# Kernel tuning notes

Hardware: AMD Instinct MI355X
Metric: run time of the kernel (lower is better)

The kernel has to match this reference:

```python
import jax, jax.numpy as jnp
import numpy as np

BF, SEQ, DIM = 8, 1024, 640
HEADS, HEAD_DIM = 8, 80
CTX, CROSS = 77, 768

def layer_norm(x, g, b, eps=1e-5):
    mu = x.mean(-1, keepdims=True)
    var = ((x - mu) ** 2).mean(-1, keepdims=True)
    return (x - mu) * jax.lax.rsqrt(var + eps) * g + b

def mha(q, k, v):
    # q: [B, Sq, DIM], k/v: [B, Sk, DIM]
    B, Sq, _ = q.shape
    scale = jnp.asarray(HEAD_DIM, q.dtype) ** -0.5
    qh = q.reshape(B, Sq, HEADS, HEAD_DIM).transpose(0, 2, 1, 3)
    kh = k.reshape(B, -1, HEADS, HEAD_DIM).transpose(0, 2, 1, 3)
    vh = v.reshape(B, -1, HEADS, HEAD_DIM).transpose(0, 2, 1, 3)
    scores = jnp.einsum('bhqd,bhkd->bhqk', qh, kh) * scale
    probs = jax.nn.softmax(scores, axis=-1)
    out = jnp.einsum('bhqk,bhkd->bhqd', probs, vh)
    return out.transpose(0, 2, 1, 3).reshape(B, Sq, HEADS * HEAD_DIM)

def sparse_causal_kv(x, f):
    # x: [(b f), d, c] -> [(b f), 2d, c]: concat frame-0 KV with previous-frame KV
    b = x.shape[0] // f
    x = x.reshape(b, f, x.shape[1], x.shape[2])
    first = jnp.broadcast_to(x[:, :1], x.shape)
    former_idx = jnp.maximum(np.arange(f) - 1, 0)
    former = x[:, former_idx]
    out = jnp.concatenate([first, former], axis=2)  # [b, f, 2d, c]
    return out.reshape(b * f, -1, x.shape[-1])


def setup_inputs() -> dict:
    key = jax.random.key(0)
    ks = jax.random.split(key, 16)
    s = lambda d: 1.0 / np.sqrt(d)
    inp = {
        'hidden_states': jax.random.normal(ks[0], (BF, SEQ, DIM), jnp.float32),
        'encoder_hidden_states': jax.random.normal(ks[1], (BF, CTX, CROSS), jnp.float32),
        'n1_g': jnp.ones((DIM,), jnp.float32), 'n1_b': jnp.zeros((DIM,), jnp.float32),
        'q1': jax.random.normal(ks[2], (DIM, DIM), jnp.float32) * s(DIM),
        'k1': jax.random.normal(ks[3], (DIM, DIM), jnp.float32) * s(DIM),
        'v1': jax.random.normal(ks[4], (DIM, DIM), jnp.float32) * s(DIM),
        'o1': jax.random.normal(ks[5], (DIM, DIM), jnp.float32) * s(DIM),
        'o1_b': jnp.zeros((DIM,), jnp.float32),
        'n2_g': jnp.ones((DIM,), jnp.float32), 'n2_b': jnp.zeros((DIM,), jnp.float32),
        'q2': jax.random.normal(ks[6], (DIM, DIM), jnp.float32) * s(DIM),
        'k2': jax.random.normal(ks[7], (CROSS, DIM), jnp.float32) * s(CROSS),
        'v2': jax.random.normal(ks[8], (CROSS, DIM), jnp.float32) * s(CROSS),
        'o2': jax.random.normal(ks[9], (DIM, DIM), jnp.float32) * s(DIM),
        'o2_b': jnp.zeros((DIM,), jnp.float32),
        'n3_g': jnp.ones((DIM,), jnp.float32), 'n3_b': jnp.zeros((DIM,), jnp.float32),
        'ff1': jax.random.normal(ks[10], (DIM, 2 * 4 * DIM), jnp.float32) * s(DIM),
        'ff1_b': jnp.zeros((2 * 4 * DIM,), jnp.float32),
        'ff2': jax.random.normal(ks[11], (4 * DIM, DIM), jnp.float32) * s(4 * DIM),
        'ff2_b': jnp.zeros((DIM,), jnp.float32),
        'video_length': 8,
    }
    return inp


def reference(hidden_states, encoder_hidden_states, n1_g, n1_b, q1, k1, v1, o1, o1_b,
              n2_g, n2_b, q2, k2, v2, o2, o2_b, n3_g, n3_b, ff1, ff1_b, ff2, ff2_b,
              video_length):
    hs = hidden_states
    # --- attn1: sparse-causal self-attention ---
    n = layer_norm(hs, n1_g, n1_b)
    q = n @ q1
    k = sparse_causal_kv(n @ k1, video_length)
    v = sparse_causal_kv(n @ v1, video_length)
    hs = mha(q, k, v) @ o1 + o1_b + hs
    # --- attn2: cross-attention to text context ---
    n = layer_norm(hs, n2_g, n2_b)
    a = mha(n @ q2, encoder_hidden_states @ k2, encoder_hidden_states @ v2)
    hs = a @ o2 + o2_b + hs
    # --- GEGLU feed-forward ---
    n = layer_norm(hs, n3_g, n3_b)
    proj = n @ ff1 + ff1_b
    x, gate = jnp.split(proj, 2, axis=-1)
    hs = (x * jax.nn.gelu(gate, approximate=False)) @ ff2 + ff2_b + hs
    return hs
```

## Files before the change

### kernel.cpp

```cpp
#include <hip/hip_runtime.h>
#include <hip/hip_bf16.h>
#include <cmath>

typedef __attribute__((ext_vector_type(8))) short short8;
typedef __attribute__((ext_vector_type(4))) short short4v;
typedef __attribute__((ext_vector_type(4))) float floatx4;

static __device__ __forceinline__ float b2f(__hip_bfloat16 x) { return __bfloat162float(x); }
static __device__ __forceinline__ __hip_bfloat16 f2b(float x) { return __float2bfloat16(x); }
static __device__ __forceinline__ short f2bs(float x) {
    __hip_bfloat16 h = __float2bfloat16(x);
    return __builtin_bit_cast(short, h);
}

static __device__ __forceinline__ float gelu_exact(float x) {
    const float z = x * 0.70710678118654752440f;
    const float a = fabsf(z);
    const float t = __frcp_rn(1.0f + 0.3275911f * a);
    float p = 1.061405429f;
    p = p * t - 1.453152027f;
    p = p * t + 1.421413741f;
    p = p * t - 0.284496736f;
    p = p * t + 0.254829592f;
    p = p * t;
    const float e = __expf(-a * a);
    float erfa = 1.0f - p * e;
    erfa = copysignf(erfa, z);
    return 0.5f * x * (1.0f + erfa);
}

static __device__ __forceinline__ void gl_lds16(const void* g, unsigned ldsoff) {
    __builtin_amdgcn_global_load_lds(
        (const __attribute__((address_space(1))) void*)(unsigned long long)(size_t)g,
        (__attribute__((address_space(3))) void*)(unsigned long long)ldsoff, 16, 0, 0);
}

__global__ void k_detect(const unsigned* __restrict__ g1, int* __restrict__ flag) {
    if (threadIdx.x == 0 && blockIdx.x == 0) {
        *flag = (*g1 == 0x3F800000u) ? 1 : 0;
    }
}

struct CvDesc { const void* src; __hip_bfloat16* dst; int n; int blk0; };
struct CvPack { CvDesc d[12]; };

__global__ __launch_bounds__(256) void k_convert_batch(CvPack P, const int* __restrict__ flag) {
    const bool isf = (*flag != 0);
    const int bid = blockIdx.x;
    int seg = 0;
#pragma unroll
    for (int i = 1; i < 12; ++i)
        if (bid >= P.d[i].blk0) seg = i;
    const CvDesc D = P.d[seg];
    const int i0 = (bid - D.blk0) * 1024 + threadIdx.x * 4;
    if (i0 >= D.n) return;
    if (isf) {
        const float* s = (const float*)D.src;
        if (i0 + 3 < D.n) {
            const float4 v = *(const float4*)(s + i0);
            short4v o4;
            o4[0] = f2bs(v.x); o4[1] = f2bs(v.y); o4[2] = f2bs(v.z); o4[3] = f2bs(v.w);
            *(short4v*)((short*)D.dst + i0) = o4;
        } else {
            for (int j = i0; j < D.n; ++j) D.dst[j] = f2b(s[j]);
        }
    } else {
        const short* s = (const short*)D.src;
        if (i0 + 3 < D.n) {
            *(short4v*)((short*)D.dst + i0) = *(const short4v*)(s + i0);
        } else {
            for (int j = i0; j < D.n; ++j) ((short*)D.dst)[j] = s[j];
        }
    }
}

struct TrDesc { const void* src; __hip_bfloat16* dst; int R; int C; int nbx; int blk0; };
struct TrPack { TrDesc d[10]; };

__global__ void k_transpose_batch(TrPack P, const int* __restrict__ flag) {
    const bool isf = (*flag != 0);
    __shared__ __hip_bfloat16 tile[32][33];
    const int bid = blockIdx.x;
    int seg = 0;
#pragma unroll
    for (int i = 1; i < 10; ++i)
        if (bid >= P.d[i].blk0) seg = i;
    const TrDesc D = P.d[seg];
    const int local = bid - D.blk0;
    const int c0 = (local % D.nbx) * 32, r0 = (local / D.nbx) * 32;
    const int tx = threadIdx.x, ty = threadIdx.y;
    for (int i = ty; i < 32; i += 8) {
        const size_t idx = (size_t)(r0 + i) * D.C + (c0 + tx);
        tile[i][tx] = isf ? f2b(((const float*)D.src)[idx]) : ((const __hip_bfloat16*)D.src)[idx];
    }
    __syncthreads();
    for (int i = ty; i < 32; i += 8)
        D.dst[(size_t)(c0 + i) * D.R + (r0 + tx)] = tile[tx][i];
}

__global__ __launch_bounds__(256) void k_layernorm(const __hip_bfloat16* __restrict__ x,
                                                   const __hip_bfloat16* __restrict__ g,
                                                   const __hip_bfloat16* __restrict__ b,
                                                   __hip_bfloat16* __restrict__ out) {
    const int w = threadIdx.x >> 6, l = threadIdx.x & 63;
    const int row = blockIdx.x * 4 + w;
    const __hip_bfloat16* xr = x + (size_t)row * 640;
    float v[10];
    float s1 = 0.f, s2 = 0.f;
#pragma unroll
    for (int i = 0; i < 10; ++i) {
        v[i] = b2f(xr[l + i * 64]);
        s1 += v[i]; s2 += v[i] * v[i];
    }
#pragma unroll
    for (int mk = 1; mk <= 32; mk <<= 1) {
        s1 += __shfl_xor(s1, mk, 64);
        s2 += __shfl_xor(s2, mk, 64);
    }
    const float mu = s1 * (1.f / 640.f);
    const float var = s2 * (1.f / 640.f) - mu * mu;
    const float rstd = rsqrtf(var + 1e-5f);
    __hip_bfloat16* orow = out + (size_t)row * 640;
#pragma unroll
    for (int i = 0; i < 10; ++i) {
        const int c = l + i * 64;
        orow[c] = f2b((v[i] - mu) * rstd * b2f(g[c]) + b2f(b[c]));
    }
}

template <int MODE>
__global__ __launch_bounds__(256, 2) void k_gemm_big(const __hip_bfloat16* __restrict__ A,
                                                     const __hip_bfloat16* __restrict__ Bt,
                                                     const __hip_bfloat16* __restrict__ bias,
                                                     const __hip_bfloat16* res,
                                                     __hip_bfloat16* outb, float* outf,
                                                     const int* __restrict__ flag,
                                                     int M, int N, int K) {
    __shared__ __align__(16) short lds[16384];
    const bool isf = (MODE == 2) ? (*flag != 0) : false;
    const int t = threadIdx.x;
    const int w = t >> 6, l = t & 63;
    const int quad = l >> 4, l16 = l & 15;
    const int wr = (w >> 1) * 64, wc = (w & 1) * 64;
    const int m0 = blockIdx.y * 128, n0 = blockIdx.x * 128;

    const int srow = t >> 2;
    const int scol = ((t & 3) ^ ((srow >> 1) & 3)) * 8;
    int ar0 = m0 + srow;       if (ar0 >= M) ar0 = M - 1;
    int ar1 = m0 + 64 + srow;  if (ar1 >= M) ar1 = M - 1;
    const __hip_bfloat16* ga0 = A + (size_t)ar0 * K + scol;
    const __hip_bfloat16* ga1 = A + (size_t)ar1 * K + scol;
    const __hip_bfloat16* gb0 = Bt + (size_t)(n0 + srow) * K + scol;
    const __hip_bfloat16* gb1 = Bt + (size_t)(n0 + 64 + srow) * K + scol;
    const unsigned ldsbase = (unsigned)(size_t)&lds[0];
    const unsigned stA0 = ldsbase + (unsigned)(w * 64) * 16;
    const unsigned stA1 = stA0 + 4096;
    const unsigned stB0 = ldsbase + 8192 + (unsigned)(w * 64) * 16;
    const unsigned stB1 = stB0 + 4096;

    const int rsw = (quad ^ ((l16 >> 1) & 3)) * 8;

    floatx4 acc[4][4];
#pragma unroll
    for (int i = 0; i < 4; ++i)
#pragma unroll
        for (int j = 0; j < 4; ++j) acc[i][j] = floatx4{0.f, 0.f, 0.f, 0.f};

    gl_lds16(ga0, stA0);
    gl_lds16(ga1, stA1);
    gl_lds16(gb0, stB0);
    gl_lds16(gb1, stB1);
    __syncthreads();

    int cur = 0;
    for (int k0 = 0; k0 < K; k0 += 32) {
        const int kn = k0 + 32;
        if (kn < K) {
            const unsigned off = (unsigned)(cur ^ 1) * 16384u;
            gl_lds16(ga0 + kn, stA0 + off);
            gl_lds16(ga1 + kn, stA1 + off);
            gl_lds16(gb0 + kn, stB0 + off);
            gl_lds16(gb1 + kn, stB1 + off);
        }
        const int cb = cur * 8192;
        short8 af[4], bf[4];
#pragma unroll
        for (int mt = 0; mt < 4; ++mt)
            af[mt] = *(const short8*)&lds[cb + (wr + mt * 16 + l16) * 32 + rsw];
#pragma unroll
        for (int nt = 0; nt < 4; ++nt)
            bf[nt] = *(const short8*)&lds[cb + 4096 + (wc + nt * 16 + l16) * 32 + rsw];
#pragma unroll
        for (int mt = 0; mt < 4; ++mt)
#pragma unroll
            for (int nt = 0; nt < 4; ++nt)
                acc[mt][nt] = __builtin_amdgcn_mfma_f32_16x16x32_bf16(af[mt], bf[nt], acc[mt][nt], 0, 0, 0);
        __syncthreads();
        cur ^= 1;
    }

#pragma unroll
    for (int mt = 0; mt < 4; ++mt)
#pragma unroll
        for (int nt = 0; nt < 4; ++nt)
#pragma unroll
            for (int r = 0; r < 4; ++r) {
                const int row = m0 + wr + mt * 16 + quad * 4 + r;
                if (row >= M) continue;
                const int col = n0 + wc + nt * 16 + l16;
                float v = acc[mt][nt][r];
                if (bias) v += b2f(bias[col]);
                const size_t idx = (size_t)row * N + col;
                if constexpr (MODE == 0) {
                    outb[idx] = f2b(v);
                } else if constexpr (MODE == 4) {
                    outb[idx] = f2b(col < 640 ? v * 0.16129851867f : v);
                } else if constexpr (MODE == 1) {
                    outb[idx] = f2b(v + b2f(res[idx]));
                } else {
                    v += b2f(res[idx]);
                    if (isf) outf[idx] = v; else outb[idx] = f2b(v);
                }
            }
}

__global__ __launch_bounds__(256, 2) void k_glu_big(const __hip_bfloat16* __restrict__ A,
                                                    const __hip_bfloat16* __restrict__ Bt,
                                                    const __hip_bfloat16* __restrict__ bias,
                                                    __hip_bfloat16* __restrict__ outp,
                                                    int M, int Nh, int K) {
    __shared__ __align__(16) short lds[24576];
    const int t = threadIdx.x;
    const int w = t >> 6, l = t & 63;
    const int quad = l >> 4, l16 = l & 15;
    const int wr = (w >> 1) * 64, wc = (w & 1) * 64;
    const int m0 = blockIdx.y * 128, n0 = blockIdx.x * 128;

    const int srow = t >> 2;
    const int scol = ((t & 3) ^ ((srow >> 1) & 3)) * 8;
    const __hip_bfloat16* ga0 = A + (size_t)(m0 + srow) * K + scol;
    const __hip_bfloat16* ga1 = A + (size_t)(m0 + 64 + srow) * K + scol;
    const __hip_bfloat16* gx0 = Bt + (size_t)(n0 + srow) * K + scol;
    const __hip_bfloat16* gx1 = Bt + (size_t)(n0 + 64 + srow) * K + scol;
    const __hip_bfloat16* gg0 = Bt + (size_t)(Nh + n0 + srow) * K + scol;
    const __hip_bfloat16* gg1 = Bt + (size_t)(Nh + n0 + 64 + srow) * K + scol;
    const unsigned ldsbase = (unsigned)(size_t)&lds[0];
    const unsigned stA0 = ldsbase + (unsigned)(w * 64) * 16;
    const unsigned stA1 = stA0 + 4096;
    const unsigned stX0 = ldsbase + 8192 + (unsigned)(w * 64) * 16;
    const unsigned stX1 = stX0 + 4096;
    const unsigned stG0 = ldsbase + 16384 + (unsigned)(w * 64) * 16;
    const unsigned stG1 = stG0 + 4096;

    const int rsw = (quad ^ ((l16 >> 1) & 3)) * 8;

    floatx4 ax[4][4], ag[4][4];
#pragma unroll
    for (int i = 0; i < 4; ++i)
#pragma unroll
        for (int j = 0; j < 4; ++j) {
            ax[i][j] = floatx4{0.f, 0.f, 0.f, 0.f};
            ag[i][j] = floatx4{0.f, 0.f, 0.f, 0.f};
        }

    gl_lds16(ga0, stA0); gl_lds16(ga1, stA1);
    gl_lds16(gx0, stX0); gl_lds16(gx1, stX1);
    gl_lds16(gg0, stG0); gl_lds16(gg1, stG1);
    __syncthreads();

    int cur = 0;
    for (int k0 = 0; k0 < K; k0 += 32) {
        const int kn = k0 + 32;
        if (kn < K) {
            const unsigned off = (unsigned)(cur ^ 1) * 24576u;
            gl_lds16(ga0 + kn, stA0 + off); gl_lds16(ga1 + kn, stA1 + off);
            gl_lds16(gx0 + kn, stX0 + off); gl_lds16(gx1 + kn, stX1 + off);
            gl_lds16(gg0 + kn, stG0 + off); gl_lds16(gg1 + kn, stG1 + off);
        }
        const int cb = cur * 12288;
        short8 af[4], bxf[4], bgf[4];
#pragma unroll
        for (int mt = 0; mt < 4; ++mt)
            af[mt] = *(const short8*)&lds[cb + (wr + mt * 16 + l16) * 32 + rsw];
#pragma unroll
        for (int nt = 0; nt < 4; ++nt) {
            bxf[nt] = *(const short8*)&lds[cb + 4096 + (wc + nt * 16 + l16) * 32 + rsw];
            bgf[nt] = *(const short8*)&lds[cb + 8192 + (wc + nt * 16 + l16) * 32 + rsw];
        }
#pragma unroll
        for (int mt = 0; mt < 4; ++mt)
#pragma unroll
            for (int nt = 0; nt < 4; ++nt) {
                ax[mt][nt] = __builtin_amdgcn_mfma_f32_16x16x32_bf16(af[mt], bxf[nt], ax[mt][nt], 0, 0, 0);
                ag[mt][nt] = __builtin_amdgcn_mfma_f32_16x16x32_bf16(af[mt], bgf[nt], ag[mt][nt], 0, 0, 0);
            }
        __syncthreads();
        cur ^= 1;
    }

#pragma unroll
    for (int mt = 0; mt < 4; ++mt)
#pragma unroll
        for (int nt = 0; nt < 4; ++nt)
#pragma unroll
            for (int r = 0; r < 4; ++r) {
                const int row = m0 + wr + mt * 16 + quad * 4 + r;
                const int col = n0 + wc + nt * 16 + l16;
                float xv = ax[mt][nt][r] + b2f(bias[col]);
                float gv = ag[mt][nt][r] + b2f(bias[Nh + col]);
                outp[(size_t)row * Nh + col] = f2b(xv * gelu_exact(gv));
            }
}

template <int MODE>
__global__ __launch_bounds__(256) void k_gemm128(const __hip_bfloat16* __restrict__ A,
                                                 const __hip_bfloat16* __restrict__ Bt,
                                                 const __hip_bfloat16* __restrict__ bias,
                                                 const __hip_bfloat16* res,
                                                 __hip_bfloat16* outb, float* outf,
                                                 const int* __restrict__ flag,
                                                 int M, int N, int K) {
    __shared__ __align__(16) short lds[12288];
    const bool isf = (MODE == 2) ? (*flag != 0) : false;
    const int t = threadIdx.x;
    const int w = t >> 6, l = t & 63;
    const int quad = l >> 4, l16 = l & 15;
    const int m0 = blockIdx.y * 128, n0 = blockIdx.x * 64;

    const int chunk = w * 64 + l;
    const int srow = chunk >> 2;
    const int scol = ((chunk & 3) ^ ((srow >> 1) & 3)) * 8;
    int ar0 = m0 + srow;       if (ar0 >= M) ar0 = M - 1;
    int ar1 = m0 + 64 + srow;  if (ar1 >= M) ar1 = M - 1;
    const __hip_bfloat16* ga0 = A + (size_t)ar0 * K + scol;
    const __hip_bfloat16* ga1 = A + (size_t)ar1 * K + scol;
    const __hip_bfloat16* gb  = Bt + (size_t)(n0 + srow) * K + scol;
    const unsigned ldsbase = (unsigned)(size_t)&lds[0];
    const unsigned stA0 = ldsbase + (unsigned)(w * 64) * 16;
    const unsigned stA1 = stA0 + 4096;
    const unsigned stB  = ldsbase + 8192 + (unsigned)(w * 64) * 16;

    const int rsw = (quad ^ ((l16 >> 1) & 3)) * 8;

    floatx4 acc[2][4];
#pragma unroll
    for (int i = 0; i < 2; ++i)
#pragma unroll
        for (int j = 0; j < 4; ++j) acc[i][j] = floatx4{0.f, 0.f, 0.f, 0.f};

    gl_lds16(ga0, stA0);
    gl_lds16(ga1, stA1);
    gl_lds16(gb, stB);
    __syncthreads();

    int cur = 0;
    for (int k0 = 0; k0 < K; k0 += 32) {
        const int kn = k0 + 32;
        if (kn < K) {
            const unsigned off = (unsigned)(cur ^ 1) * 12288u;
            gl_lds16(ga0 + kn, stA0 + off);
            gl_lds16(ga1 + kn, stA1 + off);
            gl_lds16(gb + kn, stB + off);
        }
        const int cb = cur * 6144;
        short8 af[2], bf[4];
#pragma unroll
        for (int mt = 0; mt < 2; ++mt)
            af[mt] = *(const short8*)&lds[cb + (w * 32 + mt * 16 + l16) * 32 + rsw];
#pragma unroll
        for (int nt = 0; nt < 4; ++nt)
            bf[nt] = *(const short8*)&lds[cb + 4096 + (nt * 16 + l16) * 32 + rsw];
#pragma unroll
        for (int mt = 0; mt < 2; ++mt)
#pragma unroll
            for (int nt = 0; nt < 4; ++nt)
                acc[mt][nt] = __builtin_amdgcn_mfma_f32_16x16x32_bf16(af[mt], bf[nt], acc[mt][nt], 0, 0, 0);
        __syncthreads();
        cur ^= 1;
    }

    if constexpr (MODE == 3) {
        short* vt = (short*)outb;
#pragma unroll
        for (int half = 0; half < 2; ++half) {
            __syncthreads();
#pragma unroll
            for (int nn = 0; nn < 2; ++nn) {
                const int nt = half * 2 + nn;
#pragma unroll
                for (int mt = 0; mt < 2; ++mt)
#pragma unroll
                    for (int r = 0; r < 4; ++r)
                        lds[(nn * 16 + l16) * 136 + w * 32 + mt * 16 + quad * 4 + r] =
                            f2bs(acc[mt][nt][r]);
            }
            __syncthreads();
            for (int c = t; c < 512; c += 256) {
                const int cl = c >> 4, seg = c & 15;
                const int col = n0 + half * 32 + cl;
                const int hh = col / 80, dd = col % 80;
                const int row0 = m0 + seg * 8;
                const int f = row0 >> 10, tok = row0 & 1023;
                short8 v8;
#pragma unroll
                for (int j = 0; j < 8; ++j) v8[j] = lds[cl * 136 + seg * 8 + j];
                *(short8*)(vt + (((size_t)((f * 8 + hh) * 80 + dd)) << 10) + tok) = v8;
            }
        }
        return;
    }

#pragma unroll
    for (int mt = 0; mt < 2; ++mt)
#pragma unroll
        for (int nt = 0; nt < 4; ++nt)
#pragma unroll
            for (int r = 0; r < 4; ++r) {
                const int row = m0 + w * 32 + mt * 16 + quad * 4 + r;
                if (row >= M) continue;
                const int col = n0 + nt * 16 + l16;
                float v = acc[mt][nt][r];
                if (bias) v += b2f(bias[col]);
                const size_t idx = (size_t)row * N + col;
                if constexpr (MODE == 0) {
                    outb[idx] = f2b(v);
                } else if constexpr (MODE == 1) {
                    outb[idx] = f2b(v + b2f(res[idx]));
                } else {
                    v += b2f(res[idx]);
                    if (isf) outf[idx] = v; else outb[idx] = f2b(v);
                }
            }
}

__global__ __launch_bounds__(256) void k_attn_self(const __hip_bfloat16* __restrict__ qk,
                                                   const __hip_bfloat16* __restrict__ vt,
                                                   __hip_bfloat16* __restrict__ o) {
    constexpr int KS_OFF = 0;
    constexpr int VT_OFF = 5632;
    constexpr int PS_OFF = 11712;
    constexpr int QS = 1280;
    __shared__ __align__(16) short lds[16576];
    const int t = threadIdx.x;
    const int wave = t >> 6, lane = t & 63, quad = lane >> 4, l16 = lane & 15;
    const int bid = blockIdx.x;
    const int h = bid & 7, qt = (bid >> 3) & 15, b = bid >> 7;
    const int f1 = (b > 0) ? (b - 1) : 0;
    const int nkt = (b < 2) ? 16 : 32;

    for (int i = t; i < 512; i += 256) lds[KS_OFF + (i >> 3) * 88 + 80 + (i & 7)] = 0;

    int kgo[3], klo[3], vgo[3], vlo[3];
#pragma unroll
    for (int j = 0; j < 3; ++j) {
        const int c = t + j * 256;
        const int krow = c / 10, kseg = c % 10;
        kgo[j] = krow * QS + kseg * 8;
        klo[j] = KS_OFF + krow * 88 + kseg * 8;
        const int vd = c >> 3, vseg = c & 7;
        vgo[j] = (vd << 10) + vseg * 8;
        vlo[j] = VT_OFF + vd * 76 + vseg * 8;
    }
    const int nj = (t < 128) ? 3 : 2;

    short8 qf[3];
    {
        const short* qp = (const short*)(qk + ((size_t)(b * 1024 + qt * 64 + wave * 16 + l16)) * QS + h * 80);
#pragma unroll
        for (int ks = 0; ks < 3; ++ks) {
            const int d0 = ks * 32 + quad * 8;
            qf[ks] = (d0 < 80) ? *(const short8*)(qp + d0) : short8{0, 0, 0, 0, 0, 0, 0, 0};
        }
    }

    floatx4 oacc[5];
#pragma unroll
    for (int dt = 0; dt < 5; ++dt) oacc[dt] = floatx4{0.f, 0.f, 0.f, 0.f};
    float lsum[4] = {0.f, 0.f, 0.f, 0.f};

    const short* kb0 = (const short*)qk + 640 + h * 80;
    const short* vb0 = (const short*)vt + (((size_t)h * 80) << 10);

    short8 kreg[3], vreg[3];
    {
#pragma unroll
        for (int j = 0; j < 3; ++j)
            if (j < nj) {
                kreg[j] = *(const short8*)(kb0 + kgo[j]);
                vreg[j] = *(const short8*)(vb0 + vgo[j]);
            }
#pragma unroll
        for (int j = 0; j < 3; ++j)
            if (j < nj) {
                *(short8*)&lds[klo[j]] = kreg[j];
                *(short8*)&lds[vlo[j]] = vreg[j];
            }
    }
    __syncthreads();

    for (int kt = 0; kt < nkt; ++kt) {
        const bool more = (kt + 1 < nkt);
        if (more) {
            const int kn = kt + 1;
            const int fr = (kn < 16) ? 0 : f1;
            const int tok0 = (kn < 16) ? kn * 64 : (kn - 16) * 64;
            const short* kbase = kb0 + (size_t)(fr * 1024 + tok0) * QS;
            const short* vtb = vb0 + (((size_t)(fr * 640)) << 10) + tok0;
#pragma unroll
            for (int j = 0; j < 3; ++j)
                if (j < nj) {
                    kreg[j] = *(const short8*)(kbase + kgo[j]);
                    vreg[j] = *(const short8*)(vtb + vgo[j]);
                }
        }

        floatx4 sv[4];
        __builtin_amdgcn_s_setprio(1);
#pragma unroll
        for (int nt = 0; nt < 4; ++nt) {
            floatx4 acc = {0.f, 0.f, 0.f, 0.f};
#pragma unroll
            for (int ks = 0; ks < 3; ++ks) {
                short8 bf = *(const short8*)&lds[KS_OFF + (nt * 16 + l16) * 88 + ks * 32 + quad * 8];
                acc = __builtin_amdgcn_mfma_f32_16x16x32_bf16(qf[ks], bf, acc, 0, 0, 0);
            }
            sv[nt] = acc;
        }
        __builtin_amdgcn_s_setprio(0);

#pragma unroll
        for (int nt = 0; nt < 4; ++nt) {
#pragma unroll
            for (int r = 0; r < 4; ++r) {
                const float pv = __builtin_amdgcn_exp2f(fminf(sv[nt][r], 115.f));
                lsum[r] += pv;
                lds[PS_OFF + wave * 1216 + (quad * 4 + r) * 76 + nt * 16 + l16] = f2bs(pv);
            }
        }

        __builtin_amdgcn_s_setprio(1);
#pragma unroll
        for (int ks = 0; ks < 2; ++ks) {
            short8 pf = *(const short8*)&lds[PS_OFF + wave * 1216 + l16 * 76 + ks * 32 + quad * 8];
#pragma unroll
            for (int dt = 0; dt < 5; ++dt) {
                short8 vf = *(const short8*)&lds[VT_OFF + (dt * 16 + l16) * 76 + ks * 32 + quad * 8];
                oacc[dt] = __builtin_amdgcn_mfma_f32_16x16x32_bf16(pf, vf, oacc[dt], 0, 0, 0);
            }
        }
        __builtin_amdgcn_s_setprio(0);

        if (more) {
            __syncthreads();
#pragma unroll
            for (int j = 0; j < 3; ++j)
                if (j < nj) {
                    *(short8*)&lds[klo[j]] = kreg[j];
                    *(short8*)&lds[vlo[j]] = vreg[j];
                }
            __syncthreads();
        }
    }

#pragma unroll
    for (int mk = 1; mk <= 8; mk <<= 1)
#pragma unroll
        for (int r = 0; r < 4; ++r)
            lsum[r] += __shfl_xor(lsum[r], mk, 64);

    const int orow = b * 1024 + qt * 64 + wave * 16 + quad * 4;
#pragma unroll
    for (int r = 0; r < 4; ++r) {
        const float inv = 1.f / lsum[r];
        __hip_bfloat16* op = o + (size_t)(orow + r) * 640 + h * 80 + l16;
#pragma unroll
        for (int dt = 0; dt < 5; ++dt)
            op[dt * 16] = f2b(oacc[dt][r] * inv);
    }
}

__global__ __launch_bounds__(256) void k_attn_cross(const __hip_bfloat16* __restrict__ q,
                                                    const __hip_bfloat16* __restrict__ kv,
                                                    __hip_bfloat16* __restrict__ o) {
    constexpr int KS_OFF = 0;
    constexpr int VT_OFF = 7040;
    constexpr int PS_OFF = 15360;
    __shared__ __align__(16) short lds[22016];
    const int t = threadIdx.x;
    const int wave = t >> 6, lane = t & 63, quad = lane >> 4, l16 = lane & 15;
    const int qt = blockIdx.x, h = blockIdx.y, b = blockIdx.z;
    const float scale = 0.11180339887498949f;

    for (int c = t; c < 2752; c += 256) *(short8*)&lds[c * 8] = short8{0, 0, 0, 0, 0, 0, 0, 0};
    __syncthreads();

    const short* kb = (const short*)(kv + (size_t)(b * 77) * 1280 + h * 80);
    const short* vb = (const short*)(kv + (size_t)(b * 77) * 1280 + 640 + h * 80);
    for (int c = t; c < 770; c += 256) {
        const int r = c / 10, seg = c % 10;
        *(short8*)&lds[KS_OFF + r * 88 + seg * 8] = *(const short8*)(kb + (size_t)r * 1280 + seg * 8);
        short8 v8 = *(const short8*)(vb + (size_t)r * 1280 + seg * 8);
#pragma unroll
        for (int j = 0; j < 8; ++j)
            lds[VT_OFF + (seg * 8 + j) * 104 + r] = v8[j];
    }
    short8 qf[3];
    {
        const short* qp = (const short*)(q + ((size_t)(b * 1024 + qt * 64 + wave * 16 + l16)) * 640 + h * 80);
#pragma unroll
        for (int ks = 0; ks < 3; ++ks) {
            const int d0 = ks * 32 + quad * 8;
            qf[ks] = (d0 < 80) ? *(const short8*)(qp + d0) : short8{0, 0, 0, 0, 0, 0, 0, 0};
        }
    }
    __syncthreads();

    floatx4 sv[5];
#pragma unroll
    for (int nt = 0; nt < 5; ++nt) {
        floatx4 acc = {0.f, 0.f, 0.f, 0.f};
#pragma unroll
        for (int ks = 0; ks < 3; ++ks) {
            short8 bf = *(const short8*)&lds[KS_OFF + (nt * 16 + l16) * 88 + ks * 32 + quad * 8];
            acc = __builtin_amdgcn_mfma_f32_16x16x32_bf16(qf[ks], bf, acc, 0, 0, 0);
        }
        sv[nt] = acc;
    }

    float rs[4] = {0.f, 0.f, 0.f, 0.f};
#pragma unroll
    for (int nt = 0; nt < 5; ++nt) {
#pragma unroll
        for (int r = 0; r < 4; ++r) {
            float pv = __expf(fminf(sv[nt][r] * scale, 80.f));
            if (nt == 4 && l16 >= 13) pv = 0.f;
            rs[r] += pv;
            lds[PS_OFF + wave * 1664 + (quad * 4 + r) * 104 + nt * 16 + l16] = f2bs(pv);
        }
    }
#pragma unroll
    for (int mk = 1; mk <= 8; mk <<= 1)
#pragma unroll
        for (int r = 0; r < 4; ++r)
            rs[r] += __shfl_xor(rs[r], mk, 64);

    floatx4 oacc[5];
#pragma unroll
    for (int dt = 0; dt < 5; ++dt) oacc[dt] = floatx4{0.f, 0.f, 0.f, 0.f};
#pragma unroll
    for (int ks = 0; ks < 3; ++ks) {
        short8 pf = *(const short8*)&lds[PS_OFF + wave * 1664 + l16 * 104 + ks * 32 + quad * 8];
#pragma unroll
        for (int dt = 0; dt < 5; ++dt) {
            short8 vf = *(const short8*)&lds[VT_OFF + (dt * 16 + l16) * 104 + ks * 32 + quad * 8];
            oacc[dt] = __builtin_amdgcn_mfma_f32_16x16x32_bf16(pf, vf, oacc[dt], 0, 0, 0);
        }
    }

    const int orow = b * 1024 + qt * 64 + wave * 16 + quad * 4;
#pragma unroll
    for (int r = 0; r < 4; ++r) {
        const float inv = 1.f / rs[r];
        __hip_bfloat16* op = o + (size_t)(orow + r) * 640 + h * 80 + l16;
#pragma unroll
        for (int dt = 0; dt < 5; ++dt)
            op[dt * 16] = f2b(oacc[dt][r] * inv);
    }
}

extern "C" void kernel_launch(void* const* d_in, const int* in_sizes, int n_in,
                              void* d_out, int out_size, void* d_ws, size_t ws_size,
                              hipStream_t stream) {
    char* p = (char*)d_ws;
    auto carve = [&](size_t bytes) -> void* {
        void* r = (void*)p;
        p += (bytes + 255) & ~(size_t)255;
        return r;
    };
    const size_t MD = (size_t)8192 * 640;
    int*            flag  = (int*)carve(256);
    __hip_bfloat16* resid = (__hip_bfloat16*)carve(MD * 2);
    __hip_bfloat16* nb    = (__hip_bfloat16*)carve(MD * 2);
    __hip_bfloat16* qkb   = (__hip_bfloat16*)carve((size_t)8192 * 1280 * 2);
    __hip_bfloat16* vtb   = (__hip_bfloat16*)carve((size_t)64 * 80 * 1024 * 2);
    __hip_bfloat16* ehsb  = (__hip_bfloat16*)carve((size_t)616 * 768 * 2);
    __hip_bfloat16* kvctx = (__hip_bfloat16*)carve((size_t)616 * 1280 * 2);
    __hip_bfloat16* qk1t  = (__hip_bfloat16*)carve((size_t)1280 * 640 * 2);
    __hip_bfloat16* v1t   = (__hip_bfloat16*)carve((size_t)640 * 640 * 2);
    __hip_bfloat16* kv2t  = (__hip_bfloat16*)carve((size_t)1280 * 768 * 2);
    __hip_bfloat16* q2t   = (__hip_bfloat16*)carve((size_t)640 * 640 * 2);
    __hip_bfloat16* o1t   = (__hip_bfloat16*)carve((size_t)640 * 640 * 2);
    __hip_bfloat16* o2t   = (__hip_bfloat16*)carve((size_t)640 * 640 * 2);
    __hip_bfloat16* ff1t  = (__hip_bfloat16*)carve((size_t)5120 * 640 * 2);
    __hip_bfloat16* ff2t  = (__hip_bfloat16*)carve((size_t)640 * 2560 * 2);
    __hip_bfloat16* bpool = (__hip_bfloat16*)carve((size_t)10880 * 2);
    __hip_bfloat16* n1g = bpool, *n1b = bpool + 640, *n2g = bpool + 1280, *n2b = bpool + 1920;
    __hip_bfloat16* n3g = bpool + 2560, *n3b = bpool + 3200, *o1b = bpool + 3840, *o2b = bpool + 4480;
    __hip_bfloat16* f1b = bpool + 5120, *f2b_ = bpool + 10240;

    const size_t hb_bytes = (size_t)8192 * 2560 * 2;
    __hip_bfloat16* hb = nullptr;
    {
        size_t used = (size_t)(p - (char*)d_ws);
        if (ws_size >= used + hb_bytes + 1024) hb = (__hip_bfloat16*)carve(hb_bytes);
    }

    k_detect<<<1, 64, 0, stream>>>((const unsigned*)d_in[2], flag);

    {
        CvPack P;
        auto set = [&](int i, const void* s, __hip_bfloat16* d, int n, int& blk) {
            P.d[i].src = s; P.d[i].dst = d; P.d[i].n = n; P.d[i].blk0 = blk;
            blk += (n + 1023) / 1024;
        };
        int blk = 0;
        set(0,  d_in[0],  resid, (int)MD, blk);
        set(1,  d_in[1],  ehsb, 616 * 768, blk);
        set(2,  d_in[2],  n1g, 640, blk);
        set(3,  d_in[3],  n1b, 640, blk);
        set(4,  d_in[9],  n2g, 640, blk);
        set(5,  d_in[10], n2b, 640, blk);
        set(6,  d_in[16], n3g, 640, blk);
        set(7,  d_in[17], n3b, 640, blk);
        set(8,  d_in[8],  o1b, 640, blk);
        set(9,  d_in[15], o2b, 640, blk);
        set(10, d_in[19], f1b, 5120, blk);
        set(11, d_in[21], f2b_, 640, blk);
        k_convert_batch<<<blk, 256, 0, stream>>>(P, flag);
    }

    {
        TrPack P;
        auto set = [&](int i, const void* s, __hip_bfloat16* d, int R, int C, int& blk) {
            P.d[i].src = s; P.d[i].dst = d; P.d[i].R = R; P.d[i].C = C;
            P.d[i].nbx = C / 32; P.d[i].blk0 = blk;
            blk += (C / 32) * (R / 32);
        };
        int blk = 0;
        set(0, d_in[4],  qk1t,             640, 640, blk);
        set(1, d_in[5],  qk1t + 640 * 640, 640, 640, blk);
        set(2, d_in[6],  v1t,  640, 640, blk);
        set(3, d_in[7],  o1t,  640, 640, blk);
        set(4, d_in[11], q2t,  640, 640, blk);
        set(5, d_in[12], kv2t,             768, 640, blk);
        set(6, d_in[13], kv2t + 640 * 768, 768, 640, blk);
        set(7, d_in[14], o2t,  640, 640, blk);
        set(8, d_in[18], ff1t, 640, 5120, blk);
        set(9, d_in[20], ff2t, 2560, 640, blk);
        k_transpose_batch<<<blk, dim3(32, 8), 0, stream>>>(P, flag);
    }

    k_layernorm<<<2048, 256, 0, stream>>>(resid, n1g, n1b, nb);
    k_gemm_big<4><<<dim3(10, 64), 256, 0, stream>>>(nb, qk1t, nullptr, nullptr, qkb, nullptr, flag,
                                                    8192, 1280, 640);
    k_gemm128<3><<<dim3(10, 64), 256, 0, stream>>>(nb, v1t, nullptr, nullptr, vtb, nullptr, flag,
                                                   8192, 640, 640);
    k_attn_self<<<1024, 256, 0, stream>>>(qkb, vtb, nb);
    k_gemm128<1><<<dim3(10, 64), 256, 0, stream>>>(nb, o1t, o1b, resid, resid, nullptr, flag,
                                                   8192, 640, 640);

    k_layernorm<<<2048, 256, 0, stream>>>(resid, n2g, n2b, nb);
    k_gemm128<0><<<dim3(10, 64), 256, 0, stream>>>(nb, q2t, nullptr, nullptr, qkb, nullptr, flag,
                                                   8192, 640, 640);
    k_gemm128<0><<<dim3(20, 5), 256, 0, stream>>>(ehsb, kv2t, nullptr, nullptr, kvctx, nullptr, flag,
                                                  616, 1280, 768);
    k_attn_cross<<<dim3(16, 8, 8), 256, 0, stream>>>(qkb, kvctx, nb);
    k_gemm128<1><<<dim3(10, 64), 256, 0, stream>>>(nb, o2t, o2b, resid, resid, nullptr, flag,
                                                   8192, 640, 640);

    k_layernorm<<<2048, 256, 0, stream>>>(resid, n3g, n3b, nb);
    if (hb) {
        k_glu_big<<<dim3(20, 64), 256, 0, stream>>>(nb, ff1t, f1b, hb, 8192, 2560, 640);
        k_gemm128<2><<<dim3(10, 64), 256, 0, stream>>>(hb, ff2t, f2b_, resid,
                                                       (__hip_bfloat16*)d_out, (float*)d_out, flag,
                                                       8192, 640, 2560);
    } else {
        for (int c = 0; c < 2; ++c) {
            const size_t off = (size_t)c * 4096 * 640;
            k_glu_big<<<dim3(20, 32), 256, 0, stream>>>(nb + off, ff1t, f1b, qkb, 4096, 2560, 640);
            k_gemm128<2><<<dim3(5, 32), 256, 0, stream>>>(qkb, ff2t, f2b_, resid + off,
                                                          (__hip_bfloat16*)d_out + off,
                                                          (float*)d_out + off, flag,
                                                          4096, 640, 2560);
        }
    }
    (void)in_sizes; (void)n_in; (void)out_size;
}
```

Baseline: 537.8 us.

## Split QK^T across waves by key columns and share probabilities via LDS

Each wave now holds Q fragments for all 64 query rows and computes scores against its own 16-key slice. The resulting probabilities are written to a shared LDS tile that all waves read for the PV product. Row sums are combined across waves through LDS before normalisation. This cuts per-wave K fragment loads from LDS, but adds a block barrier per key tile and quadruples the Q register footprint.

```diff
diff --git a/kernel.cpp b/kernel.cpp
--- a/kernel.cpp
+++ b/kernel.cpp
@@ -463,20 +463,26 @@
     }
     const int nj = (t < 128) ? 3 : 2;
 
-    short8 qf[3];
-    {
-        const short* qp = (const short*)(qk + ((size_t)(b * 1024 + qt * 64 + wave * 16 + l16)) * QS + h * 80);
+    short8 qf[4][3];
+#pragma unroll
+    for (int g = 0; g < 4; ++g) {
+        const short* qp = (const short*)(qk +
+            ((size_t)(b * 1024 + qt * 64 + g * 16 + l16)) * QS + h * 80);
 #pragma unroll
         for (int ks = 0; ks < 3; ++ks) {
             const int d0 = ks * 32 + quad * 8;
-            qf[ks] = (d0 < 80) ? *(const short8*)(qp + d0) : short8{0, 0, 0, 0, 0, 0, 0, 0};
+            qf[g][ks] = (d0 < 80) ? *(const short8*)(qp + d0) : short8{0, 0, 0, 0, 0, 0, 0, 0};
         }
     }
 
     floatx4 oacc[5];
 #pragma unroll
     for (int dt = 0; dt < 5; ++dt) oacc[dt] = floatx4{0.f, 0.f, 0.f, 0.f};
-    float lsum[4] = {0.f, 0.f, 0.f, 0.f};
+    float lsum[4][4];
+#pragma unroll
+    for (int g = 0; g < 4; ++g)
+#pragma unroll
+        for (int r = 0; r < 4; ++r) lsum[g][r] = 0.f;
 
     const short* kb0 = (const short*)qk + 640 + h * 80;
     const short* vb0 = (const short*)vt + (((size_t)h * 80) << 10);
@@ -514,34 +520,33 @@
                 }
         }
 
-        floatx4 sv[4];
+        short8 kf[3];
+#pragma unroll
+        for (int ks = 0; ks < 3; ++ks)
+            kf[ks] = *(const short8*)&lds[KS_OFF + (wave * 16 + l16) * 88 + ks * 32 + quad * 8];
+
         __builtin_amdgcn_s_setprio(1);
 #pragma unroll
-        for (int nt = 0; nt < 4; ++nt) {
+        for (int g = 0; g < 4; ++g) {
             floatx4 acc = {0.f, 0.f, 0.f, 0.f};
 #pragma unroll
-            for (int ks = 0; ks < 3; ++ks) {
-                short8 bf = *(const short8*)&lds[KS_OFF + (nt * 16 + l16) * 88 + ks * 32 + quad * 8];
-                acc = __builtin_amdgcn_mfma_f32_16x16x32_bf16(qf[ks], bf, acc, 0, 0, 0);
-            }
-            sv[nt] = acc;
+            for (int ks = 0; ks < 3; ++ks)
+                acc = __builtin_amdgcn_mfma_f32_16x16x32_bf16(qf[g][ks], kf[ks], acc, 0, 0, 0);
+#pragma unroll
+            for (int r = 0; r < 4; ++r) {
+                const float pv = __builtin_amdgcn_exp2f(fminf(acc[r], 115.f));
+                lsum[g][r] += pv;
+                lds[PS_OFF + (g * 16 + quad * 4 + r) * 76 + wave * 16 + l16] = f2bs(pv);
+            }
         }
         __builtin_amdgcn_s_setprio(0);
 
-#pragma unroll
-        for (int nt = 0; nt < 4; ++nt) {
-#pragma unroll
-            for (int r = 0; r < 4; ++r) {
-                const float pv = __builtin_amdgcn_exp2f(fminf(sv[nt][r], 115.f));
-                lsum[r] += pv;
-                lds[PS_OFF + wave * 1216 + (quad * 4 + r) * 76 + nt * 16 + l16] = f2bs(pv);
-            }
-        }
+        __syncthreads();
 
         __builtin_amdgcn_s_setprio(1);
 #pragma unroll
         for (int ks = 0; ks < 2; ++ks) {
-            short8 pf = *(const short8*)&lds[PS_OFF + wave * 1216 + l16 * 76 + ks * 32 + quad * 8];
+            short8 pf = *(const short8*)&lds[PS_OFF + (wave * 16 + l16) * 76 + ks * 32 + quad * 8];
 #pragma unroll
             for (int dt = 0; dt < 5; ++dt) {
                 short8 vf = *(const short8*)&lds[VT_OFF + (dt * 16 + l16) * 76 + ks * 32 + quad * 8];
@@ -565,13 +570,27 @@
 #pragma unroll
     for (int mk = 1; mk <= 8; mk <<= 1)
 #pragma unroll
-        for (int r = 0; r < 4; ++r)
-            lsum[r] += __shfl_xor(lsum[r], mk, 64);
+        for (int g = 0; g < 4; ++g)
+#pragma unroll
+            for (int r = 0; r < 4; ++r)
+                lsum[g][r] += __shfl_xor(lsum[g][r], mk, 64);
+
+    float* fls = (float*)lds;
+    if (l16 == 0) {
+#pragma unroll
+        for (int g = 0; g < 4; ++g)
+#pragma unroll
+            for (int r = 0; r < 4; ++r)
+                fls[wave * 64 + g * 16 + quad * 4 + r] = lsum[g][r];
+    }
+    __syncthreads();
 
     const int orow = b * 1024 + qt * 64 + wave * 16 + quad * 4;
 #pragma unroll
     for (int r = 0; r < 4; ++r) {
-        const float inv = 1.f / lsum[r];
+        const int q = wave * 16 + quad * 4 + r;
+        const float tot = fls[q] + fls[64 + q] + fls[128 + q] + fls[192 + q];
+        const float inv = 1.f / tot;
         __hip_bfloat16* op = o + (size_t)(orow + r) * 640 + h * 80 + l16;
 #pragma unroll
         for (int dt = 0; dt < 5; ++dt)
```

New measurement: 539.5 us. Within noise of the previous version (+0.3%).
